# Optimization experiments

Measured on AMD Instinct MI355X. Metric: run time of the kernel, lower is better.

Reference implementation:

```python
import jax, jax.numpy as jnp
import numpy as np

BN_EPS = 1e-5


def setup_inputs() -> dict:
    key = jax.random.key(0)
    ks = jax.random.split(key, 6)
    B, C, K, N = 4, 64, 16, 16384  # batch, feat channels, neighbors, points
    W_OUT = 16  # weightnet output channels (fixed by Linear(16*mlp[-1], ...))
    xyz = jax.random.normal(ks[0], (B, N, 3), dtype=jnp.float32)
    points = jax.random.normal(ks[1], (B, C, K, N), dtype=jnp.float32)
    coordinate = jax.random.normal(ks[2], (B, 3, K, N), dtype=jnp.float32)
    w1 = jax.random.normal(ks[3], (W_OUT, 3), dtype=jnp.float32) * 0.5
    b1 = jnp.zeros((W_OUT,), dtype=jnp.float32)
    lin_w = jax.random.normal(ks[4], (C, W_OUT * C), dtype=jnp.float32) * (1.0 / np.sqrt(W_OUT * C))
    lin_b = jnp.zeros((C,), dtype=jnp.float32)
    gamma = jnp.ones((C,), dtype=jnp.float32)
    beta = jnp.zeros((C,), dtype=jnp.float32)
    return {"xyz": xyz, "points": points, "coordinate": coordinate,
            "w1": w1, "b1": b1, "lin_w": lin_w, "lin_b": lin_b,
            "gamma": gamma, "beta": beta}


def reference(xyz, points, coordinate, w1, b1, lin_w, lin_b, gamma, beta):
    B, C, K, N = points.shape
    # weightnet: 1x1 conv (3 -> 16) + ReLU over coordinate [B,3,K,N] -> [B,16,K,N]
    weights = jax.nn.relu(jnp.einsum('oc,bckn->bokn', w1, coordinate) + b1[None, :, None, None])
    # per-point aggregation: [B,N,C,K] @ [B,N,K,16] -> [B,N,C,16]
    new_points = jnp.einsum('bckn,bokn->bnco', points, weights)
    new_points = new_points.reshape(B, N, C * 16)  # [B, N, 16*C]
    # linear projection 16*C -> C
    new_points = jnp.einsum('bnk,ok->bno', new_points, lin_w) + lin_b  # [B, N, C]
    # BatchNorm1d over channel dim (training-mode batch stats), layout [B, C, N]
    new_points = new_points.transpose(0, 2, 1)  # [B, C, N]
    mean = jnp.mean(new_points, axis=(0, 2), keepdims=True)
    var = jnp.var(new_points, axis=(0, 2), keepdims=True)
    new_points = (new_points - mean) * jax.lax.rsqrt(var + BN_EPS)
    new_points = new_points * gamma[None, :, None] + beta[None, :, None]
    new_points = jax.nn.relu(new_points)  # [B, C, N]
    return (xyz, new_points)
```

## Files before the change

### kernel.cpp

```cpp
#include <hip/hip_runtime.h>

#define BB 4
#define CC 64
#define KK 16
#define NN 16384
#define NTB 128

typedef __attribute__((ext_vector_type(8))) short short8;
typedef __attribute__((ext_vector_type(4))) float floatx4;
typedef __attribute__((ext_vector_type(2))) _Float16 half2v;

__device__ __forceinline__ unsigned short f2bf_rtne(float x) {
    unsigned u = __builtin_bit_cast(unsigned, x);
    u += 0x7FFFu + ((u >> 16) & 1u);
    return (unsigned short)(u >> 16);
}

__device__ __forceinline__ unsigned pack_bf16x2(float lo, float hi) {
    unsigned a = __builtin_bit_cast(unsigned, lo) + 0x8000u;
    unsigned b = __builtin_bit_cast(unsigned, hi) + 0x8000u;
    return __builtin_amdgcn_perm(b, a, 0x07060302u);
}

__device__ __forceinline__ half2v cvt2h(float a, float b) {
    return __builtin_bit_cast(half2v, __builtin_amdgcn_cvt_pkrtz(a, b));
}

#if __has_builtin(__builtin_amdgcn_fdot2)
#define DOT2(a, b, c) __builtin_amdgcn_fdot2((a), (b), (c), false)
#else
__device__ __forceinline__ float dot2_fb(half2v a, half2v b, float c) {
    return fmaf((float)a[0], (float)b[0], fmaf((float)a[1], (float)b[1], c));
}
#define DOT2(a, b, c) dot2_fb((a), (b), (c))
#endif

__global__ __launch_bounds__(256)
void prep_bfrag(const float* __restrict__ lin_w, unsigned short* __restrict__ bfrag)
{
    const int tid  = blockIdx.x * 256 + threadIdx.x;
    const int lane = tid & 63;
    const int g    = tid >> 6;
    const int ci   = g >> 4;
    const int kk   = (g >> 2) & 3;
    const int nt   = g & 3;
    const int r    = lane & 15;
    const int sq   = lane >> 4;

    const float* src = lin_w + (size_t)(nt * 16 + r) * 1024 + ci * 128 + kk * 32 + sq * 8;
    unsigned short v[8];
    #pragma unroll
    for (int j = 0; j < 8; ++j) v[j] = f2bf_rtne(src[j]);
    *(uint4*)(bfrag + ((size_t)g * 64 + lane) * 8) = *(const uint4*)v;
}

__global__ __launch_bounds__(256, 2)
void fused_main(const float* __restrict__ points,
                const float* __restrict__ coordinate,
                const float* __restrict__ w1,
                const float* __restrict__ b1,
                const unsigned short* __restrict__ bfrag,
                float* __restrict__ y_out)
{
    __shared__ uint4 s_a[2][2][4 * 257];

    const int t    = threadIdx.x;
    const int lane = t & 63;
    const int wv   = __builtin_amdgcn_readfirstlane(t >> 6);
    const int P    = wv >> 1;
    const int h    = wv & 1;
    const int r    = lane & 15;
    const int sq   = lane >> 4;

    const int bid = blockIdx.x;
    const int b   = bid >> 7;
    const int n0  = (bid & 127) * NTB + P * 64;

    half2v wh[8][8];
    {
        const float* coordB = coordinate + (size_t)b * 3 * KK * NN + n0 + lane;
        float c0[KK], c1[KK], c2[KK];
        #pragma unroll
        for (int k = 0; k < KK; ++k) {
            c0[k] = coordB[(0 * KK + k) * NN];
            c1[k] = coordB[(1 * KK + k) * NN];
            c2[k] = coordB[(2 * KK + k) * NN];
        }
        #pragma unroll
        for (int j = 0; j < 8; ++j) {
            const int o = 8 * h + j;
            const float w1x = w1[o * 3 + 0];
            const float w1y = w1[o * 3 + 1];
            const float w1z = w1[o * 3 + 2];
            const float bo  = b1[o];
            #pragma unroll
            for (int kp = 0; kp < 8; ++kp) {
                float v0 = fmaf(w1x, c0[2 * kp],     fmaf(w1y, c1[2 * kp],     fmaf(w1z, c2[2 * kp],     bo)));
                float v1 = fmaf(w1x, c0[2 * kp + 1], fmaf(w1y, c1[2 * kp + 1], fmaf(w1z, c2[2 * kp + 1], bo)));
                wh[j][kp] = cvt2h(fmaxf(v0, 0.0f), fmaxf(v1, 0.0f));
            }
        }
    }

    floatx4 acc[2][4];
    #pragma unroll
    for (int m = 0; m < 2; ++m)
        #pragma unroll
        for (int nt = 0; nt < 4; ++nt) acc[m][nt] = (floatx4){0.f, 0.f, 0.f, 0.f};

    const float* pB = points + (size_t)b * CC * KK * NN + n0 + lane;

    float pv[4][16];
    #pragma unroll
    for (int d = 0; d < 4; ++d)
        #pragma unroll
        for (int k = 0; k < KK; ++k)
            pv[d][k] = pB[((size_t)d * KK + k) * NN];

#define CHANNEL_SECTION(CARG)                                                   \
    {                                                                           \
        const int c_ = (CARG);                                                  \
        uint4* saW = &s_a[P][c_ & 1][0];                                        \
        _Pragma("unroll")                                                       \
        for (int cl = 0; cl < 8; ++cl) {                                        \
            const int cc   = c_ * 8 + cl;                                       \
            const int slot = cl & 3;                   \
            half2v ph[8];                                                       \
            _Pragma("unroll")                                                   \
            for (int kp = 0; kp < 8; ++kp)                                      \
                ph[kp] = cvt2h(pv[slot][2 * kp], pv[slot][2 * kp + 1]);         \
            {                                                                   \
                const int cp = (cc + 4 < CC) ? (cc + 4) : (CC - 1);             \
                _Pragma("unroll")                                               \
                for (int k = 0; k < KK; ++k)                                    \
                    pv[slot][k] = pB[((size_t)cp * KK + k) * NN];               \
            }                                                                   \
            float a8[8];                                                        \
            _Pragma("unroll")                                                   \
            for (int j = 0; j < 8; ++j) {                                       \
                float a = 0.f;                                                  \
                _Pragma("unroll")                                               \
                for (int kp = 0; kp < 8; ++kp) a = DOT2(ph[kp], wh[j][kp], a);  \
                a8[j] = a;                                                      \
            }                                                                   \
            uint4 pk;                                                           \
            pk.x = pack_bf16x2(a8[0], a8[1]);                                   \
            pk.y = pack_bf16x2(a8[2], a8[3]);                                   \
            pk.z = pack_bf16x2(a8[4], a8[5]);                                   \
            pk.w = pack_bf16x2(a8[6], a8[7]);                                   \
            saW[(lane >> 4) * 257 + (cl >> 1) * 64 + (lane & 15) * 4            \
                + (cl & 1) * 2 + h] = pk;                                       \
        }                                                                       \
    }

    CHANNEL_SECTION(0)

    uint4 bf_c[4];
    #pragma unroll
    for (int nt = 0; nt < 4; ++nt)
        bf_c[nt] = *(const uint4*)(bfrag + ((((size_t)0 * 4 + 0) * 4 + nt) * 64 + lane) * 8);

    asm volatile("s_waitcnt lgkmcnt(0)\n\ts_barrier" ::: "memory");

    for (int ci = 0; ci < 8; ++ci) {
        if (ci < 7) CHANNEL_SECTION(ci + 1)

        const uint4* saR = &s_a[P][ci & 1][0];
        #pragma unroll
        for (int kk = 0; kk < 4; ++kk) {
            uint4 bf_n[4];
            if (kk < 3) {
                #pragma unroll
                for (int nt = 0; nt < 4; ++nt)
                    bf_n[nt] = *(const uint4*)(bfrag + ((((size_t)ci * 4 + kk + 1) * 4 + nt) * 64 + lane) * 8);
            }
            short8 af[2];
            #pragma unroll
            for (int m = 0; m < 2; ++m)
                af[m] = __builtin_bit_cast(short8, saR[(2 * h + m) * 257 + kk * 64 + r * 4 + sq]);
            #pragma unroll
            for (int m = 0; m < 2; ++m)
                #pragma unroll
                for (int nt = 0; nt < 4; ++nt)
                    acc[m][nt] = __builtin_amdgcn_mfma_f32_16x16x32_bf16(
                        af[m], __builtin_bit_cast(short8, bf_c[nt]), acc[m][nt], 0, 0, 0);
            #pragma unroll
            for (int nt = 0; nt < 4; ++nt) bf_c[nt] = bf_n[nt];
        }

        if (ci < 7) {
            #pragma unroll
            for (int nt = 0; nt < 4; ++nt)
                bf_c[nt] = *(const uint4*)(bfrag + ((((size_t)(ci + 1) * 4 + 0) * 4 + nt) * 64 + lane) * 8);
            asm volatile("s_waitcnt lgkmcnt(0)\n\ts_barrier" ::: "memory");
        }
    }
#undef CHANNEL_SECTION

    float* yB = y_out + (size_t)b * CC * NN + n0;
    #pragma unroll
    for (int m = 0; m < 2; ++m)
        #pragma unroll
        for (int nt = 0; nt < 4; ++nt) {
            const int oc = nt * 16 + r;
            const float4 v = make_float4(acc[m][nt][0], acc[m][nt][1],
                                         acc[m][nt][2], acc[m][nt][3]);
            *(float4*)(yB + (size_t)oc * NN + (2 * h + m) * 16 + sq * 4) = v;
        }
}

__global__ __launch_bounds__(256)
void bn_reduce(const float* __restrict__ y, float* __restrict__ part)
{
    const int ch = blockIdx.x & 63;
    const int b  = blockIdx.x >> 6;
    const int t  = threadIdx.x;
    const float4* p = (const float4*)(y + ((size_t)b * CC + ch) * NN);
    float s = 0.f, ss = 0.f;
    for (int i = t; i < NN / 4; i += 256) {
        const float4 v = p[i];
        s  += v.x + v.y + v.z + v.w;
        ss += v.x * v.x + v.y * v.y + v.z * v.z + v.w * v.w;
    }
    #pragma unroll
    for (int m = 1; m < 64; m <<= 1) {
        s  += __shfl_xor(s, m);
        ss += __shfl_xor(ss, m);
    }
    __shared__ float rs[4], rss[4];
    if ((t & 63) == 0) { rs[t >> 6] = s; rss[t >> 6] = ss; }
    __syncthreads();
    if (t == 0) {
        part[blockIdx.x]       = rs[0] + rs[1] + rs[2] + rs[3];
        part[256 + blockIdx.x] = rss[0] + rss[1] + rss[2] + rss[3];
    }
}

__global__ void bn_stats(const float* __restrict__ part,
                         const float* __restrict__ gamma,
                         const float* __restrict__ beta,
                         float* __restrict__ ab)
{
    const int ch = threadIdx.x;
    float S = 0.f, SS = 0.f;
    #pragma unroll
    for (int b = 0; b < BB; ++b) {
        S  += part[b * 64 + ch];
        SS += part[256 + b * 64 + ch];
    }
    const float inv  = 1.0f / (float)(BB * NN);
    const float mean = S * inv;
    const float var  = SS * inv - mean * mean;
    const float a    = gamma[ch] * rsqrtf(var + 1e-5f);
    ab[ch]      = a;
    ab[CC + ch] = beta[ch] - mean * a;
}

__global__ __launch_bounds__(256)
void bn_apply(float* __restrict__ y, const float* __restrict__ ab)
{
    const size_t i = (size_t)blockIdx.x * 256 + threadIdx.x;
    float4* p = (float4*)y;
    float4 v = p[i];
    const int ch = (int)((i * 4) >> 14) & 63;
    const float a = ab[ch], bb = ab[CC + ch];
    v.x = fmaxf(fmaf(a, v.x, bb), 0.0f);
    v.y = fmaxf(fmaf(a, v.y, bb), 0.0f);
    v.z = fmaxf(fmaf(a, v.z, bb), 0.0f);
    v.w = fmaxf(fmaf(a, v.w, bb), 0.0f);
    p[i] = v;
}

extern "C" void kernel_launch(void* const* d_in, const int* in_sizes, int n_in,
                              void* d_out, int out_size, void* d_ws, size_t ws_size,
                              hipStream_t stream)
{
    const float* xyz        = (const float*)d_in[0];
    const float* points     = (const float*)d_in[1];
    const float* coordinate = (const float*)d_in[2];
    const float* w1         = (const float*)d_in[3];
    const float* b1         = (const float*)d_in[4];
    const float* lin_w      = (const float*)d_in[5];
    const float* gamma      = (const float*)d_in[7];
    const float* beta       = (const float*)d_in[8];

    float* out = (float*)d_out;

    unsigned short* bfrag = (unsigned short*)d_ws;
    float* part = (float*)d_ws + 32768;
    float* ab   = part + 512;

    const size_t xyz_elems = (size_t)BB * NN * 3;
    (void)hipMemcpyAsync(out, xyz, xyz_elems * sizeof(float),
                         hipMemcpyDeviceToDevice, stream);

    float* y_out = out + xyz_elems;

    prep_bfrag<<<32, 256, 0, stream>>>(lin_w, bfrag);
    fused_main<<<BB * (NN / NTB), 256, 0, stream>>>(
        points, coordinate, w1, b1, bfrag, y_out);
    bn_reduce<<<BB * CC, 256, 0, stream>>>(y_out, part);
    bn_stats<<<1, 64, 0, stream>>>(part, gamma, beta, ab);
    bn_apply<<<(BB * CC * NN) / 4 / 256, 256, 0, stream>>>(y_out, ab);
}
```

Before: 413.1 us.

## Fuse BN statistics into main kernel via atomics and shrink point tile per block

Removes the separate bn_reduce pass by computing per-channel sum and sum-of-squares in the fused_main epilogue and accumulating them with atomicAdd into a buffer zeroed in prep_bfrag. Halves the points per block (64 instead of 128) so each of the four waves owns 4 weightnet outputs and one M-tile, cutting registers and shared memory and raising the occupancy hint to 3. Point values are converted to half on load to shrink register storage. This adds global atomics and changes the floating-point summation order.

```diff
diff --git a/kernel.cpp b/kernel.cpp
--- a/kernel.cpp
+++ b/kernel.cpp
@@ -4,7 +4,7 @@
 #define CC 64
 #define KK 16
 #define NN 16384
-#define NTB 128
+#define NTB 64
 
 typedef __attribute__((ext_vector_type(8))) short short8;
 typedef __attribute__((ext_vector_type(4))) float floatx4;
@@ -36,9 +36,12 @@
 #endif
 
 __global__ __launch_bounds__(256)
-void prep_bfrag(const float* __restrict__ lin_w, unsigned short* __restrict__ bfrag)
+void prep_bfrag(const float* __restrict__ lin_w, unsigned short* __restrict__ bfrag,
+                float* __restrict__ part)
 {
     const int tid  = blockIdx.x * 256 + threadIdx.x;
+    if (tid < 512) part[tid] = 0.0f;
+
     const int lane = tid & 63;
     const int g    = tid >> 6;
     const int ci   = g >> 4;
@@ -54,29 +57,28 @@
     *(uint4*)(bfrag + ((size_t)g * 64 + lane) * 8) = *(const uint4*)v;
 }
 
-__global__ __launch_bounds__(256, 2)
+__global__ __launch_bounds__(256, 3)
 void fused_main(const float* __restrict__ points,
                 const float* __restrict__ coordinate,
                 const float* __restrict__ w1,
                 const float* __restrict__ b1,
                 const unsigned short* __restrict__ bfrag,
-                float* __restrict__ y_out)
-{
-    __shared__ uint4 s_a[2][2][4 * 257];
+                float* __restrict__ y_out,
+                float* __restrict__ part)
+{
+    __shared__ uint4 s_a[2][4 * 257];
 
     const int t    = threadIdx.x;
     const int lane = t & 63;
-    const int wv   = __builtin_amdgcn_readfirstlane(t >> 6);
-    const int P    = wv >> 1;
-    const int h    = wv & 1;
+    const int w    = __builtin_amdgcn_readfirstlane(t >> 6);
     const int r    = lane & 15;
     const int sq   = lane >> 4;
 
     const int bid = blockIdx.x;
-    const int b   = bid >> 7;
-    const int n0  = (bid & 127) * NTB + P * 64;
-
-    half2v wh[8][8];
+    const int b   = bid >> 8;
+    const int n0  = (bid & 255) * NTB;
+
+    half2v wh[4][8];
     {
         const float* coordB = coordinate + (size_t)b * 3 * KK * NN + n0 + lane;
         float c0[KK], c1[KK], c2[KK];
@@ -87,8 +89,8 @@
             c2[k] = coordB[(2 * KK + k) * NN];
         }
         #pragma unroll
-        for (int j = 0; j < 8; ++j) {
-            const int o = 8 * h + j;
+        for (int j = 0; j < 4; ++j) {
+            const int o = 4 * w + j;
             const float w1x = w1[o * 3 + 0];
             const float w1y = w1[o * 3 + 1];
             const float w1z = w1[o * 3 + 2];
@@ -102,54 +104,50 @@
         }
     }
 
-    floatx4 acc[2][4];
-    #pragma unroll
-    for (int m = 0; m < 2; ++m)
-        #pragma unroll
-        for (int nt = 0; nt < 4; ++nt) acc[m][nt] = (floatx4){0.f, 0.f, 0.f, 0.f};
+    floatx4 acc[4];
+    #pragma unroll
+    for (int nt = 0; nt < 4; ++nt) acc[nt] = (floatx4){0.f, 0.f, 0.f, 0.f};
 
     const float* pB = points + (size_t)b * CC * KK * NN + n0 + lane;
 
-    float pv[4][16];
+    half2v pv[4][8];
     #pragma unroll
     for (int d = 0; d < 4; ++d)
         #pragma unroll
-        for (int k = 0; k < KK; ++k)
-            pv[d][k] = pB[((size_t)d * KK + k) * NN];
+        for (int i = 0; i < 8; ++i)
+            pv[d][i] = cvt2h(pB[((size_t)(d * KK + 2 * i))     * NN],
+                             pB[((size_t)(d * KK + 2 * i + 1)) * NN]);
 
 #define CHANNEL_SECTION(CARG)                                                   \
     {                                                                           \
         const int c_ = (CARG);                                                  \
-        uint4* saW = &s_a[P][c_ & 1][0];                                        \
+        uint4* saW = &s_a[c_ & 1][0];                                           \
         _Pragma("unroll")                                                       \
         for (int cl = 0; cl < 8; ++cl) {                                        \
             const int cc   = c_ * 8 + cl;                                       \
             const int slot = cl & 3;                   \
-            half2v ph[8];                                                       \
+            float a8[4];                                                        \
             _Pragma("unroll")                                                   \
-            for (int kp = 0; kp < 8; ++kp)                                      \
-                ph[kp] = cvt2h(pv[slot][2 * kp], pv[slot][2 * kp + 1]);         \
+            for (int j = 0; j < 4; ++j) {                                       \
+                float a = 0.f;                                                  \
+                _Pragma("unroll")                                               \
+                for (int kp = 0; kp < 8; ++kp) a = DOT2(pv[slot][kp], wh[j][kp], a); \
+                a8[j] = a;                                                      \
+            }                                                                   \
             {                                                                   \
                 const int cp = (cc + 4 < CC) ? (cc + 4) : (CC - 1);             \
                 _Pragma("unroll")                                               \
-                for (int k = 0; k < KK; ++k)                                    \
-                    pv[slot][k] = pB[((size_t)cp * KK + k) * NN];               \
+                for (int i = 0; i < 8; ++i)                                     \
+                    pv[slot][i] = cvt2h(pB[((size_t)(cp * KK + 2 * i))     * NN], \
+                                        pB[((size_t)(cp * KK + 2 * i + 1)) * NN]); \
             }                                                                   \
-            float a8[8];                                                        \
-            _Pragma("unroll")                                                   \
-            for (int j = 0; j < 8; ++j) {                                       \
-                float a = 0.f;                                                  \
-                _Pragma("unroll")                                               \
-                for (int kp = 0; kp < 8; ++kp) a = DOT2(ph[kp], wh[j][kp], a);  \
-                a8[j] = a;                                                      \
-            }                                                                   \
-            uint4 pk;                                                           \
+            uint2 pk;                                                           \
             pk.x = pack_bf16x2(a8[0], a8[1]);                                   \
             pk.y = pack_bf16x2(a8[2], a8[3]);                                   \
-            pk.z = pack_bf16x2(a8[4], a8[5]);                                   \
-            pk.w = pack_bf16x2(a8[6], a8[7]);                                   \
-            saW[(lane >> 4) * 257 + (cl >> 1) * 64 + (lane & 15) * 4            \
-                + (cl & 1) * 2 + h] = pk;                                       \
+            uint2* dst = (uint2*)&saW[(lane >> 4) * 257 + (cl >> 1) * 64        \
+                                      + (lane & 15) * 4 + (cl & 1) * 2          \
+                                      + (w >> 1)] + (w & 1);                    \
+            *dst = pk;                                                          \
         }                                                                       \
     }
 
@@ -165,7 +163,7 @@
     for (int ci = 0; ci < 8; ++ci) {
         if (ci < 7) CHANNEL_SECTION(ci + 1)
 
-        const uint4* saR = &s_a[P][ci & 1][0];
+        const uint4* saR = &s_a[ci & 1][0];
         #pragma unroll
         for (int kk = 0; kk < 4; ++kk) {
             uint4 bf_n[4];
@@ -174,16 +172,11 @@
                 for (int nt = 0; nt < 4; ++nt)
                     bf_n[nt] = *(const uint4*)(bfrag + ((((size_t)ci * 4 + kk + 1) * 4 + nt) * 64 + lane) * 8);
             }
-            short8 af[2];
-            #pragma unroll
-            for (int m = 0; m < 2; ++m)
-                af[m] = __builtin_bit_cast(short8, saR[(2 * h + m) * 257 + kk * 64 + r * 4 + sq]);
-            #pragma unroll
-            for (int m = 0; m < 2; ++m)
-                #pragma unroll
-                for (int nt = 0; nt < 4; ++nt)
-                    acc[m][nt] = __builtin_amdgcn_mfma_f32_16x16x32_bf16(
-                        af[m], __builtin_bit_cast(short8, bf_c[nt]), acc[m][nt], 0, 0, 0);
+            const short8 af = __builtin_bit_cast(short8, saR[w * 257 + kk * 64 + r * 4 + sq]);
+            #pragma unroll
+            for (int nt = 0; nt < 4; ++nt)
+                acc[nt] = __builtin_amdgcn_mfma_f32_16x16x32_bf16(
+                    af, __builtin_bit_cast(short8, bf_c[nt]), acc[nt], 0, 0, 0);
             #pragma unroll
             for (int nt = 0; nt < 4; ++nt) bf_c[nt] = bf_n[nt];
         }
@@ -199,40 +192,19 @@
 
     float* yB = y_out + (size_t)b * CC * NN + n0;
     #pragma unroll
-    for (int m = 0; m < 2; ++m)
-        #pragma unroll
-        for (int nt = 0; nt < 4; ++nt) {
-            const int oc = nt * 16 + r;
-            const float4 v = make_float4(acc[m][nt][0], acc[m][nt][1],
-                                         acc[m][nt][2], acc[m][nt][3]);
-            *(float4*)(yB + (size_t)oc * NN + (2 * h + m) * 16 + sq * 4) = v;
-        }
-}
-
-__global__ __launch_bounds__(256)
-void bn_reduce(const float* __restrict__ y, float* __restrict__ part)
-{
-    const int ch = blockIdx.x & 63;
-    const int b  = blockIdx.x >> 6;
-    const int t  = threadIdx.x;
-    const float4* p = (const float4*)(y + ((size_t)b * CC + ch) * NN);
-    float s = 0.f, ss = 0.f;
-    for (int i = t; i < NN / 4; i += 256) {
-        const float4 v = p[i];
-        s  += v.x + v.y + v.z + v.w;
-        ss += v.x * v.x + v.y * v.y + v.z * v.z + v.w * v.w;
-    }
-    #pragma unroll
-    for (int m = 1; m < 64; m <<= 1) {
-        s  += __shfl_xor(s, m);
-        ss += __shfl_xor(ss, m);
-    }
-    __shared__ float rs[4], rss[4];
-    if ((t & 63) == 0) { rs[t >> 6] = s; rss[t >> 6] = ss; }
-    __syncthreads();
-    if (t == 0) {
-        part[blockIdx.x]       = rs[0] + rs[1] + rs[2] + rs[3];
-        part[256 + blockIdx.x] = rss[0] + rss[1] + rss[2] + rss[3];
+    for (int nt = 0; nt < 4; ++nt) {
+        const int oc = nt * 16 + r;
+        const float4 v = make_float4(acc[nt][0], acc[nt][1], acc[nt][2], acc[nt][3]);
+        *(float4*)(yB + (size_t)oc * NN + w * 16 + sq * 4) = v;
+
+        float s  = v.x + v.y + v.z + v.w;
+        float ss = v.x * v.x + v.y * v.y + v.z * v.z + v.w * v.w;
+        s  += __shfl_xor(s, 16);  s  += __shfl_xor(s, 32);
+        ss += __shfl_xor(ss, 16); ss += __shfl_xor(ss, 32);
+        if (lane < 16) {
+            atomicAdd(&part[b * 64 + oc], s);
+            atomicAdd(&part[256 + b * 64 + oc], ss);
+        }
     }
 }
 
@@ -296,10 +268,9 @@
 
     float* y_out = out + xyz_elems;
 
-    prep_bfrag<<<32, 256, 0, stream>>>(lin_w, bfrag);
+    prep_bfrag<<<32, 256, 0, stream>>>(lin_w, bfrag, part);
     fused_main<<<BB * (NN / NTB), 256, 0, stream>>>(
-        points, coordinate, w1, b1, bfrag, y_out);
-    bn_reduce<<<BB * CC, 256, 0, stream>>>(y_out, part);
+        points, coordinate, w1, b1, bfrag, y_out, part);
     bn_stats<<<1, 64, 0, stream>>>(part, gamma, beta, ab);
     bn_apply<<<(BB * CC * NN) / 4 / 256, 256, 0, stream>>>(y_out, ab);
 }
```

Result: slower. 749.9 us (+81.5%).

## Fuse BatchNorm statistics reduction into main kernel epilogue with atomics

Applied to the files above, without the earlier changes.

The main kernel now computes per-channel sum and sum-of-squares from its output tile in registers. It reduces them with shuffles and shared memory, then atomically adds them into a partial buffer that prep_bfrag zeroes. This removes the separate bn_reduce pass, which re-read the whole intermediate output. The channel loop is also restructured so the weighting computation for a chunk is no longer overlapped with the MFMA work of the previous chunk, which may lose latency hiding while simplifying register use.

```diff
diff --git a/kernel.cpp b/kernel.cpp
--- a/kernel.cpp
+++ b/kernel.cpp
@@ -36,9 +36,12 @@
 #endif
 
 __global__ __launch_bounds__(256)
-void prep_bfrag(const float* __restrict__ lin_w, unsigned short* __restrict__ bfrag)
+void prep_bfrag(const float* __restrict__ lin_w, unsigned short* __restrict__ bfrag,
+                float* __restrict__ part)
 {
     const int tid  = blockIdx.x * 256 + threadIdx.x;
+    if (tid < 512) part[tid] = 0.0f;
+
     const int lane = tid & 63;
     const int g    = tid >> 6;
     const int ci   = g >> 4;
@@ -60,7 +63,8 @@
                 const float* __restrict__ w1,
                 const float* __restrict__ b1,
                 const unsigned short* __restrict__ bfrag,
-                float* __restrict__ y_out)
+                float* __restrict__ y_out,
+                float* __restrict__ part)
 {
     __shared__ uint4 s_a[2][2][4 * 257];
 
@@ -117,55 +121,47 @@
         for (int k = 0; k < KK; ++k)
             pv[d][k] = pB[((size_t)d * KK + k) * NN];
 
-#define CHANNEL_SECTION(CARG)                                                   \
-    {                                                                           \
-        const int c_ = (CARG);                                                  \
-        uint4* saW = &s_a[P][c_ & 1][0];                                        \
-        _Pragma("unroll")                                                       \
-        for (int cl = 0; cl < 8; ++cl) {                                        \
-            const int cc   = c_ * 8 + cl;                                       \
-            const int slot = cl & 3;                   \
-            half2v ph[8];                                                       \
-            _Pragma("unroll")                                                   \
-            for (int kp = 0; kp < 8; ++kp)                                      \
-                ph[kp] = cvt2h(pv[slot][2 * kp], pv[slot][2 * kp + 1]);         \
-            {                                                                   \
-                const int cp = (cc + 4 < CC) ? (cc + 4) : (CC - 1);             \
-                _Pragma("unroll")                                               \
-                for (int k = 0; k < KK; ++k)                                    \
-                    pv[slot][k] = pB[((size_t)cp * KK + k) * NN];               \
-            }                                                                   \
-            float a8[8];                                                        \
-            _Pragma("unroll")                                                   \
-            for (int j = 0; j < 8; ++j) {                                       \
-                float a = 0.f;                                                  \
-                _Pragma("unroll")                                               \
-                for (int kp = 0; kp < 8; ++kp) a = DOT2(ph[kp], wh[j][kp], a);  \
-                a8[j] = a;                                                      \
-            }                                                                   \
-            uint4 pk;                                                           \
-            pk.x = pack_bf16x2(a8[0], a8[1]);                                   \
-            pk.y = pack_bf16x2(a8[2], a8[3]);                                   \
-            pk.z = pack_bf16x2(a8[4], a8[5]);                                   \
-            pk.w = pack_bf16x2(a8[6], a8[7]);                                   \
-            saW[(lane >> 4) * 257 + (cl >> 1) * 64 + (lane & 15) * 4            \
-                + (cl & 1) * 2 + h] = pk;                                       \
-        }                                                                       \
-    }
-
-    CHANNEL_SECTION(0)
-
-    uint4 bf_c[4];
-    #pragma unroll
-    for (int nt = 0; nt < 4; ++nt)
-        bf_c[nt] = *(const uint4*)(bfrag + ((((size_t)0 * 4 + 0) * 4 + nt) * 64 + lane) * 8);
-
-    asm volatile("s_waitcnt lgkmcnt(0)\n\ts_barrier" ::: "memory");
-
     for (int ci = 0; ci < 8; ++ci) {
-        if (ci < 7) CHANNEL_SECTION(ci + 1)
-
-        const uint4* saR = &s_a[P][ci & 1][0];
+        const int buf = ci & 1;
+        uint4* saW = &s_a[P][buf][0];
+        #pragma unroll
+        for (int cl = 0; cl < 8; ++cl) {
+            const int cc   = ci * 8 + cl;
+            const int slot = cc & 3;
+            half2v ph[8];
+            #pragma unroll
+            for (int kp = 0; kp < 8; ++kp)
+                ph[kp] = cvt2h(pv[slot][2 * kp], pv[slot][2 * kp + 1]);
+            {
+                const int cp = (cc + 4 < CC) ? (cc + 4) : (CC - 1);
+                #pragma unroll
+                for (int k = 0; k < KK; ++k)
+                    pv[slot][k] = pB[((size_t)cp * KK + k) * NN];
+            }
+            float a8[8];
+            #pragma unroll
+            for (int j = 0; j < 8; ++j) {
+                float a = 0.f;
+                #pragma unroll
+                for (int kp = 0; kp < 8; ++kp) a = DOT2(ph[kp], wh[j][kp], a);
+                a8[j] = a;
+            }
+            uint4 pk;
+            pk.x = pack_bf16x2(a8[0], a8[1]);
+            pk.y = pack_bf16x2(a8[2], a8[3]);
+            pk.z = pack_bf16x2(a8[4], a8[5]);
+            pk.w = pack_bf16x2(a8[6], a8[7]);
+            saW[(lane >> 4) * 257 + (cl >> 1) * 64 + (lane & 15) * 4 + (cl & 1) * 2 + h] = pk;
+        }
+
+        uint4 bf_c[4];
+        #pragma unroll
+        for (int nt = 0; nt < 4; ++nt)
+            bf_c[nt] = *(const uint4*)(bfrag + ((((size_t)ci * 4 + 0) * 4 + nt) * 64 + lane) * 8);
+
+        asm volatile("s_waitcnt lgkmcnt(0)\n\ts_barrier" ::: "memory");
+
+        const uint4* saR = &s_a[P][buf][0];
         #pragma unroll
         for (int kk = 0; kk < 4; ++kk) {
             uint4 bf_n[4];
@@ -187,17 +183,11 @@
             #pragma unroll
             for (int nt = 0; nt < 4; ++nt) bf_c[nt] = bf_n[nt];
         }
-
-        if (ci < 7) {
-            #pragma unroll
-            for (int nt = 0; nt < 4; ++nt)
-                bf_c[nt] = *(const uint4*)(bfrag + ((((size_t)(ci + 1) * 4 + 0) * 4 + nt) * 64 + lane) * 8);
-            asm volatile("s_waitcnt lgkmcnt(0)\n\ts_barrier" ::: "memory");
-        }
-    }
-#undef CHANNEL_SECTION
+    }
 
     float* yB = y_out + (size_t)b * CC * NN + n0;
+    float* sb  = (float*)&s_a[0][0][0];
+    float* sb2 = sb + 512;
     #pragma unroll
     for (int m = 0; m < 2; ++m)
         #pragma unroll
@@ -206,33 +196,26 @@
             const float4 v = make_float4(acc[m][nt][0], acc[m][nt][1],
                                          acc[m][nt][2], acc[m][nt][3]);
             *(float4*)(yB + (size_t)oc * NN + (2 * h + m) * 16 + sq * 4) = v;
-        }
-}
-
-__global__ __launch_bounds__(256)
-void bn_reduce(const float* __restrict__ y, float* __restrict__ part)
-{
-    const int ch = blockIdx.x & 63;
-    const int b  = blockIdx.x >> 6;
-    const int t  = threadIdx.x;
-    const float4* p = (const float4*)(y + ((size_t)b * CC + ch) * NN);
-    float s = 0.f, ss = 0.f;
-    for (int i = t; i < NN / 4; i += 256) {
-        const float4 v = p[i];
-        s  += v.x + v.y + v.z + v.w;
-        ss += v.x * v.x + v.y * v.y + v.z * v.z + v.w * v.w;
-    }
-    #pragma unroll
-    for (int m = 1; m < 64; m <<= 1) {
-        s  += __shfl_xor(s, m);
-        ss += __shfl_xor(ss, m);
-    }
-    __shared__ float rs[4], rss[4];
-    if ((t & 63) == 0) { rs[t >> 6] = s; rss[t >> 6] = ss; }
+
+            float s  = v.x + v.y + v.z + v.w;
+            float ss = v.x * v.x + v.y * v.y + v.z * v.z + v.w * v.w;
+            s  += __shfl_xor(s, 16);  s  += __shfl_xor(s, 32);
+            ss += __shfl_xor(ss, 16); ss += __shfl_xor(ss, 32);
+            if (lane < 16) {
+                sb [(wv * 2 + m) * 64 + oc] = s;
+                sb2[(wv * 2 + m) * 64 + oc] = ss;
+            }
+        }
     __syncthreads();
-    if (t == 0) {
-        part[blockIdx.x]       = rs[0] + rs[1] + rs[2] + rs[3];
-        part[256 + blockIdx.x] = rss[0] + rss[1] + rss[2] + rss[3];
+    if (t < 64) {
+        float S = 0.f, SS = 0.f;
+        #pragma unroll
+        for (int q = 0; q < 8; ++q) {
+            S  += sb [q * 64 + t];
+            SS += sb2[q * 64 + t];
+        }
+        atomicAdd(&part[b * 64 + t], S);
+        atomicAdd(&part[256 + b * 64 + t], SS);
     }
 }
 
@@ -296,10 +279,9 @@
 
     float* y_out = out + xyz_elems;
 
-    prep_bfrag<<<32, 256, 0, stream>>>(lin_w, bfrag);
+    prep_bfrag<<<32, 256, 0, stream>>>(lin_w, bfrag, part);
     fused_main<<<BB * (NN / NTB), 256, 0, stream>>>(
-        points, coordinate, w1, b1, bfrag, y_out);
-    bn_reduce<<<BB * CC, 256, 0, stream>>>(y_out, part);
+        points, coordinate, w1, b1, bfrag, y_out, part);
     bn_stats<<<1, 64, 0, stream>>>(part, gamma, beta, ab);
     bn_apply<<<(BB * CC * NN) / 4 / 256, 256, 0, stream>>>(y_out, ab);
 }
```

After: 400.5 us. -3.1%, faster.
